# Kernel optimization log

Hardware: AMD Instinct MI355X
Metric: run time of the kernel (lower is better)

The kernel has to match this reference:

```python
import jax, jax.numpy as jnp
import numpy as np

B, S, H, DH = 2, 2048, 12, 64
D = H * DH          # dim_hidden = 768
DF = 4 * D          # dim_ffn = 3072
EPS = 1e-5


def layernorm(x, g, b):
    mu = jnp.mean(x, -1, keepdims=True)
    var = jnp.var(x, -1, keepdims=True)
    return (x - mu) * jax.lax.rsqrt(var + EPS) * g + b


def setup_inputs() -> dict:
    key = jax.random.key(0)
    ks = jax.random.split(key, 8)
    sc = 0.02
    x = jax.random.normal(ks[0], (B, S, D), jnp.float32)
    # causal mask: True where attention is NOT allowed (masked_fill semantics)
    causal = ~jnp.tril(jnp.ones((S, S), dtype=bool))
    attn_mask = jnp.broadcast_to(causal, (B, S, S))
    Wq = jax.random.normal(ks[1], (D, D), jnp.float32) * sc
    Wk = jax.random.normal(ks[2], (D, D), jnp.float32) * sc
    Wv = jax.random.normal(ks[3], (D, D), jnp.float32) * sc
    Wo = jax.random.normal(ks[4], (D, D), jnp.float32) * sc
    bo = jnp.zeros((D,), jnp.float32)
    g1 = jnp.ones((D,), jnp.float32)
    b1 = jnp.zeros((D,), jnp.float32)
    W1 = jax.random.normal(ks[5], (DF, D), jnp.float32) * sc  # conv1 (k=1) == linear
    bb1 = jnp.zeros((DF,), jnp.float32)
    W2 = jax.random.normal(ks[6], (D, DF), jnp.float32) * sc
    bb2 = jnp.zeros((D,), jnp.float32)
    g2 = jnp.ones((D,), jnp.float32)
    b2 = jnp.zeros((D,), jnp.float32)
    return dict(x=x, attn_mask=attn_mask, Wq=Wq, Wk=Wk, Wv=Wv, Wo=Wo, bo=bo,
                g1=g1, b1=b1, W1=W1, bb1=bb1, W2=W2, bb2=bb2, g2=g2, b2=b2)


def reference(x, attn_mask, Wq, Wk, Wv, Wo, bo, g1, b1, W1, bb1, W2, bb2, g2, b2):
    b, s, d = x.shape
    # projections and head split: (B, H, S, DH)
    q = (x @ Wq.T).reshape(b, s, H, DH).transpose(0, 2, 1, 3)
    k = (x @ Wk.T).reshape(b, s, H, DH).transpose(0, 2, 1, 3)
    v = (x @ Wv.T).reshape(b, s, H, DH).transpose(0, 2, 1, 3)
    scores = jnp.einsum('bhqd,bhkd->bhqk', q, k) / jnp.sqrt(jnp.float32(DH))
    scores = jnp.where(attn_mask[:, None, :, :], jnp.float32(-1e9), scores)
    attn_p = jax.nn.softmax(scores, axis=-1)          # (B, H, S, S)
    attn_v = jnp.einsum('bhqk,bhkd->bhqd', attn_p, v)
    attn_v = attn_v.transpose(0, 2, 1, 3).reshape(b, s, d)
    attn_out = attn_v @ Wo.T + bo
    h = layernorm(x + attn_out, g1, b1)
    f = jax.nn.gelu(h @ W1.T + bb1, approximate=False) @ W2.T + bb2
    y = layernorm(h + f, g2, b2)
    return y, attn_p
```

## Files before the change

### kernel.cpp

```cpp
#include <hip/hip_runtime.h>
#include <hip/hip_bf16.h>

#define DEV static __device__ __forceinline__

typedef short bf16x8  __attribute__((ext_vector_type(8)));
typedef short short4v __attribute__((ext_vector_type(4)));
typedef float f32x4   __attribute__((ext_vector_type(4)));

#define MFMA16(a,b,c) __builtin_amdgcn_mfma_f32_16x16x32_bf16((a),(b),(c),0,0,0)

DEV short f2b(float f) {
  unsigned u = __float_as_uint(f);
  unsigned r = (u + 0x7fffu + ((u >> 16) & 1u)) >> 16;
  return (short)r;
}

DEV void gld16(const void* g, void* l) {
  __builtin_amdgcn_global_load_lds(
      (const __attribute__((address_space(1))) unsigned int*)g,
      (__attribute__((address_space(3))) unsigned int*)l, 16, 0, 0);
}

DEV bf16x8 ldfrag(const short* tile, int row, int unit) {
  return *(const bf16x8*)(tile + row * 64 + (((unit) ^ (row & 7)) << 3));
}

__global__ __launch_bounds__(256) void cast4(const float4* __restrict__ in,
                                             short4v* __restrict__ out, int n4) {
  int i = blockIdx.x * 256 + threadIdx.x;
  if (i < n4) {
    float4 v = in[i];
    short4v o;
    o[0] = f2b(v.x); o[1] = f2b(v.y); o[2] = f2b(v.z); o[3] = f2b(v.w);
    out[i] = o;
  }
}

__global__ __launch_bounds__(256) void cast4_m(
    const float4* __restrict__ s0, const float4* __restrict__ s1,
    const float4* __restrict__ s2, const float4* __restrict__ s3,
    short4v* __restrict__ d0, short4v* __restrict__ d1,
    short4v* __restrict__ d2, short4v* __restrict__ d3, int n4) {
  int i = blockIdx.x * 256 + threadIdx.x;
  if (i >= n4) return;
  int b = blockIdx.y;
  const float4* s = (b == 0) ? s0 : (b == 1) ? s1 : (b == 2) ? s2 : s3;
  short4v* d = (b == 0) ? d0 : (b == 1) ? d1 : (b == 2) ? d2 : d3;
  float4 v = s[i];
  short4v o;
  o[0] = f2b(v.x); o[1] = f2b(v.y); o[2] = f2b(v.z); o[3] = f2b(v.w);
  d[i] = o;
}

template <int MODE>
__global__ __launch_bounds__(256) void gemm_nt(
    const short* __restrict__ A, const short* __restrict__ Bw,
    float* __restrict__ outF, short* __restrict__ outB,
    short* __restrict__ outB2, short* __restrict__ outB3,
    const float* __restrict__ bias, int M, int N, int K, int Kstride,
    float scale) {
  __shared__ __align__(16) short As[128 * 64];
  __shared__ __align__(16) short Bs[128 * 64];
  int tid = threadIdx.x;
  int w = tid >> 6, lane = tid & 63, quad = lane >> 4, l15 = lane & 15;
  int m0 = blockIdx.x * 128, n0 = blockIdx.y * 128;
  int kbase = blockIdx.z * K;
  const short* Ap = A + kbase;
  const short* Bp = Bw + kbase;
  int wm = (w & 1) * 64, wn = (w >> 1) * 64;
  f32x4 acc[4][4] = {};

  for (int k0 = 0; k0 < K; k0 += 64) {
    __syncthreads();
#pragma unroll
    for (int i = 0; i < 4; i++) {
      int id = i * 256 + tid;
      int r = id >> 3, u = id & 7;
      int su = u ^ (r & 7);
      gld16(Ap + (size_t)(m0 + r) * Kstride + k0 + su * 8, As + id * 8);
      gld16(Bp + (size_t)(n0 + r) * Kstride + k0 + su * 8, Bs + id * 8);
    }
    __syncthreads();
#pragma unroll
    for (int kk = 0; kk < 2; kk++) {
      bf16x8 af[4], bfr[4];
#pragma unroll
      for (int mt = 0; mt < 4; mt++)
        af[mt] = ldfrag(As, wm + mt * 16 + l15, kk * 4 + quad);
#pragma unroll
      for (int nt = 0; nt < 4; nt++)
        bfr[nt] = ldfrag(Bs, wn + nt * 16 + l15, kk * 4 + quad);
#pragma unroll
      for (int mt = 0; mt < 4; mt++)
#pragma unroll
        for (int nt = 0; nt < 4; nt++)
          acc[mt][nt] = MFMA16(af[mt], bfr[nt], acc[mt][nt]);
    }
  }

  if (MODE == 0) outF += (size_t)blockIdx.z * M * N;

#pragma unroll
  for (int mt = 0; mt < 4; mt++) {
#pragma unroll
    for (int nt = 0; nt < 4; nt++) {
      if (MODE == 4 && n0 >= 1536) {
        int gcol = n0 + wn + nt * 16 + l15;
        int col = gcol - 1536;
        int h_ = col >> 6, d_ = col & 63;
        int srow = m0 + wm + mt * 16 + quad * 4;
        int b_ = srow >> 11, s_ = srow & 2047;
        short4v pk;
#pragma unroll
        for (int reg = 0; reg < 4; reg++) pk[reg] = f2b(acc[mt][nt][reg]);
        *(short4v*)(outB3 + ((size_t)(b_ * 12 + h_) * 64 + d_) * 2048 + s_) = pk;
      } else {
#pragma unroll
        for (int reg = 0; reg < 4; reg++) {
          int grow = m0 + wm + mt * 16 + quad * 4 + reg;
          int gcol = n0 + wn + nt * 16 + l15;
          float v = acc[mt][nt][reg];
          if (MODE == 0) {
            outF[(size_t)grow * N + gcol] = v;
          } else if (MODE == 3) {
            float t = v + bias[gcol];
            float z = t * (1.0f + 0.044715f * t * t);
            float ge = t / (1.0f + __expf(-1.5957691216f * z));
            outB[(size_t)grow * N + gcol] = f2b(ge);
          } else if (MODE == 4) {
            int b_ = grow >> 11, s_ = grow & 2047;
            if (gcol < 768) {
              int h_ = gcol >> 6, d_ = gcol & 63;
              outB[(((size_t)(b_ * 12 + h_) << 11) + s_) * 64 + d_] = f2b(v * scale);
            } else {
              int col = gcol - 768;
              int h_ = col >> 6, d_ = col & 63;
              outB2[(((size_t)(b_ * 12 + h_) << 11) + s_) * 64 + d_] = f2b(v);
            }
          }
        }
      }
    }
  }
}

__global__ __launch_bounds__(256) void attn_kernel(
    const short* __restrict__ Qb, const short* __restrict__ Kb,
    const short* __restrict__ Vtb, float* __restrict__ Pout,
    short* __restrict__ Ov) {
  __shared__ __align__(16) short Qs[64 * 64];
  __shared__ __align__(16) short Ks[64 * 64];
  __shared__ __align__(16) short Vs[64 * 64];
  __shared__ __align__(16) short Ps[4 * 16 * 64];
  int tid = threadIdx.x, w = tid >> 6, lane = tid & 63;
  int quad = lane >> 4, l15 = lane & 15;
  int qb = (gridDim.x - 1) - blockIdx.x;
  int bh = blockIdx.y, q0 = qb << 6;
  const short* qp = Qb + ((size_t)bh << 17);
  const short* kp = Kb + ((size_t)bh << 17);
  const short* vp = Vtb + ((size_t)bh << 17);
  float* pp = Pout + ((size_t)bh << 22);

#pragma unroll
  for (int t = 0; t < 2; t++) {
    int row = t * 32 + w * 8 + (lane >> 3);
    int su = (lane & 7) ^ (row & 7);
    gld16(qp + ((size_t)(q0 + row) << 6) + su * 8, Qs + row * 64 + (lane & 7) * 8);
  }

  float lsum[4] = {0.f, 0.f, 0.f, 0.f};

  for (int kt = 0; kt <= qb; kt++) {
    __syncthreads();
#pragma unroll
    for (int t = 0; t < 2; t++) {
      int row = t * 32 + w * 8 + (lane >> 3);
      int su = (lane & 7) ^ (row & 7);
      gld16(kp + ((size_t)((kt << 6) + row) << 6) + su * 8,
            Ks + row * 64 + (lane & 7) * 8);
    }
    __syncthreads();
    f32x4 sc[4] = {};
    int arow = w * 16 + l15;
    bf16x8 a0 = ldfrag(Qs, arow, quad), a1 = ldfrag(Qs, arow, 4 + quad);
#pragma unroll
    for (int nt = 0; nt < 4; nt++) {
      int brow = nt * 16 + l15;
      bf16x8 b0 = ldfrag(Ks, brow, quad), b1 = ldfrag(Ks, brow, 4 + quad);
      sc[nt] = MFMA16(a0, b0, sc[nt]);
      sc[nt] = MFMA16(a1, b1, sc[nt]);
    }
    if (kt == qb) {
#pragma unroll
      for (int nt = 0; nt < 4; nt++) {
        int key = (kt << 6) + nt * 16 + l15;
#pragma unroll
        for (int reg = 0; reg < 4; reg++) {
          int qg = q0 + w * 16 + quad * 4 + reg;
          if (key > qg) sc[nt][reg] = -1e30f;
        }
      }
    }
#pragma unroll
    for (int reg = 0; reg < 4; reg++)
      lsum[reg] += __expf(sc[0][reg]) + __expf(sc[1][reg]) +
                   __expf(sc[2][reg]) + __expf(sc[3][reg]);
  }

  float rl[4];
#pragma unroll
  for (int reg = 0; reg < 4; reg++) {
    float s = lsum[reg];
#pragma unroll
    for (int xm = 1; xm < 16; xm <<= 1) s += __shfl_xor(s, xm, 64);
    rl[reg] = 1.0f / s;
  }
  f32x4 oacc[4] = {};

  for (int kt = 0; kt <= qb; kt++) {
    __syncthreads();
#pragma unroll
    for (int t = 0; t < 2; t++) {
      int row = t * 32 + w * 8 + (lane >> 3);
      int su = (lane & 7) ^ (row & 7);
      gld16(kp + ((size_t)((kt << 6) + row) << 6) + su * 8,
            Ks + row * 64 + (lane & 7) * 8);
      gld16(vp + (size_t)row * 2048 + (kt << 6) + su * 8,
            Vs + row * 64 + (lane & 7) * 8);
    }
    __syncthreads();
    f32x4 sc[4] = {};
    int arow = w * 16 + l15;
    bf16x8 a0 = ldfrag(Qs, arow, quad), a1 = ldfrag(Qs, arow, 4 + quad);
#pragma unroll
    for (int nt = 0; nt < 4; nt++) {
      int brow = nt * 16 + l15;
      bf16x8 b0 = ldfrag(Ks, brow, quad), b1 = ldfrag(Ks, brow, 4 + quad);
      sc[nt] = MFMA16(a0, b0, sc[nt]);
      sc[nt] = MFMA16(a1, b1, sc[nt]);
    }
    if (kt == qb) {
#pragma unroll
      for (int nt = 0; nt < 4; nt++) {
        int key = (kt << 6) + nt * 16 + l15;
#pragma unroll
        for (int reg = 0; reg < 4; reg++) {
          int qg = q0 + w * 16 + quad * 4 + reg;
          if (key > qg) sc[nt][reg] = -1e30f;
        }
      }
    }
#pragma unroll
    for (int nt = 0; nt < 4; nt++) {
      int key = (kt << 6) + nt * 16 + l15;
#pragma unroll
      for (int reg = 0; reg < 4; reg++) {
        int qg = q0 + w * 16 + quad * 4 + reg;
        float p = __expf(sc[nt][reg]) * rl[reg];
        pp[((size_t)qg << 11) + key] = p;
        int prow = quad * 4 + reg, pcol = nt * 16 + l15;
        Ps[(w << 10) + prow * 64 + (((pcol >> 3) ^ (prow & 7)) << 3) + (pcol & 7)] =
            f2b(p);
      }
    }
    bf16x8 p0 = ldfrag(Ps + (w << 10), l15, quad);
    bf16x8 p1 = ldfrag(Ps + (w << 10), l15, 4 + quad);
#pragma unroll
    for (int dn = 0; dn < 4; dn++) {
      int vrow = dn * 16 + l15;
      bf16x8 v0 = ldfrag(Vs, vrow, quad), v1 = ldfrag(Vs, vrow, 4 + quad);
      oacc[dn] = MFMA16(p0, v0, oacc[dn]);
      oacc[dn] = MFMA16(p1, v1, oacc[dn]);
    }
  }

  int b_ = bh / 12, h_ = bh - b_ * 12;
#pragma unroll
  for (int dn = 0; dn < 4; dn++)
#pragma unroll
    for (int reg = 0; reg < 4; reg++) {
      int s_ = q0 + w * 16 + quad * 4 + reg;
      Ov[(size_t)((b_ << 11) + s_) * 768 + h_ * 64 + dn * 16 + l15] =
          f2b(oacc[dn][reg]);
    }

  int kstart = (qb + 1) << 6;
  if (kstart < 2048) {
    int nch = (2048 - kstart) >> 2;
    for (int r = 0; r < 64; r++) {
      float4* dst = (float4*)(pp + ((size_t)(q0 + r) << 11) + kstart);
      for (int c = tid; c < nch; c += 256) dst[c] = make_float4(0.f, 0.f, 0.f, 0.f);
    }
  }
}

template <int NP>
__global__ __launch_bounds__(256) void ln_fuse(
    const float* __restrict__ p0, const float* __restrict__ p1,
    const float* __restrict__ p2, const float* __restrict__ p3,
    const float* __restrict__ resid, const float* __restrict__ bias,
    const float* __restrict__ gw, const float* __restrict__ bw,
    float* __restrict__ outF, short* __restrict__ outB) {
  int row = blockIdx.x, tid = threadIdx.x;
  size_t off = (size_t)row * 768;
  float v[3];
#pragma unroll
  for (int i = 0; i < 3; i++) {
    int col = tid + i * 256;
    float t = p0[off + col] + resid[off + col] + bias[col];
    if (NP > 1) t += p1[off + col];
    if (NP > 2) t += p2[off + col];
    if (NP > 3) t += p3[off + col];
    v[i] = t;
  }
  float s = v[0] + v[1] + v[2];
  float ss = v[0] * v[0] + v[1] * v[1] + v[2] * v[2];
#pragma unroll
  for (int xm = 1; xm < 64; xm <<= 1) {
    s += __shfl_xor(s, xm, 64);
    ss += __shfl_xor(ss, xm, 64);
  }
  __shared__ float red[8];
  int w = tid >> 6, lane = tid & 63;
  if (lane == 0) { red[w] = s; red[w + 4] = ss; }
  __syncthreads();
  s = red[0] + red[1] + red[2] + red[3];
  ss = red[4] + red[5] + red[6] + red[7];
  float mu = s * (1.0f / 768.0f);
  float var = ss * (1.0f / 768.0f) - mu * mu;
  float inv = rsqrtf(var + 1e-5f);
  float* yF = outF + off;
#pragma unroll
  for (int i = 0; i < 3; i++) {
    int col = tid + i * 256;
    float y = (v[i] - mu) * inv * gw[col] + bw[col];
    yF[col] = y;
    if (outB) outB[off + col] = f2b(y);
  }
}

extern "C" void kernel_launch(void* const* d_in, const int* in_sizes, int n_in,
                              void* d_out, int out_size, void* d_ws, size_t ws_size,
                              hipStream_t stream) {
  const float* x  = (const float*)d_in[0];
  const float* Wq = (const float*)d_in[2];
  const float* Wk = (const float*)d_in[3];
  const float* Wv = (const float*)d_in[4];
  const float* Wo = (const float*)d_in[5];
  const float* bo = (const float*)d_in[6];
  const float* g1 = (const float*)d_in[7];
  const float* b1 = (const float*)d_in[8];
  const float* W1 = (const float*)d_in[9];
  const float* bb1 = (const float*)d_in[10];
  const float* W2 = (const float*)d_in[11];
  const float* bb2 = (const float*)d_in[12];
  const float* g2 = (const float*)d_in[13];
  const float* b2 = (const float*)d_in[14];

  const size_t P = (size_t)4096 * 768;

  char* cur = (char*)d_ws;
  auto take = [&](size_t n) { char* p = cur; cur += (n + 255) & ~(size_t)255; return p; };
  short* xb   = (short*)take(P * 2);
  short* wqkv = (short*)take((size_t)2304 * 768 * 2);
  short* wob  = (short*)take((size_t)589824 * 2);
  short* w1b  = (short*)take((size_t)2359296 * 2);
  short* w2b  = (short*)take((size_t)2359296 * 2);
  short* qbf  = (short*)take(P * 2);
  short* kbf  = (short*)take(P * 2);
  short* vtb  = (short*)take(P * 2);
  short* avb  = (short*)take(P * 2);
  short* hb   = (short*)take(P * 2);
  short* ub   = (short*)take((size_t)4096 * 3072 * 2);
  float* t1   = (float*)take(P * 2 * 4);
  float* hf   = (float*)take(P * 4);
  float* t2   = (float*)take(P * 4 * 4);

  float* y_out = (float*)d_out;
  float* p_out = (float*)d_out + P;

  cast4<<<3072, 256, 0, stream>>>((const float4*)x, (short4v*)xb, 786432);
  cast4_m<<<dim3(576, 4), 256, 0, stream>>>(
      (const float4*)Wq, (const float4*)Wk, (const float4*)Wv, (const float4*)Wo,
      (short4v*)wqkv, (short4v*)(wqkv + 589824), (short4v*)(wqkv + 1179648),
      (short4v*)wob, 147456);
  cast4_m<<<dim3(2304, 2), 256, 0, stream>>>(
      (const float4*)W1, (const float4*)W2, (const float4*)W1, (const float4*)W2,
      (short4v*)w1b, (short4v*)w2b, (short4v*)w1b, (short4v*)w2b, 589824);

  gemm_nt<4><<<dim3(32, 18), 256, 0, stream>>>(
      xb, wqkv, nullptr, qbf, kbf, vtb, nullptr, 4096, 2304, 768, 768, 0.125f);
  attn_kernel<<<dim3(32, 24), 256, 0, stream>>>(qbf, kbf, vtb, p_out, avb);
  gemm_nt<0><<<dim3(32, 6, 2), 256, 0, stream>>>(
      avb, wob, t1, nullptr, nullptr, nullptr, nullptr, 4096, 768, 384, 768, 1.0f);
  ln_fuse<2><<<4096, 256, 0, stream>>>(t1, t1 + P, nullptr, nullptr, x, bo,
                                       g1, b1, hf, hb);
  gemm_nt<3><<<dim3(32, 24), 256, 0, stream>>>(
      hb, w1b, nullptr, ub, nullptr, nullptr, bb1, 4096, 3072, 768, 768, 1.0f);
  gemm_nt<0><<<dim3(32, 6, 4), 256, 0, stream>>>(
      ub, w2b, t2, nullptr, nullptr, nullptr, nullptr, 4096, 768, 768, 3072, 1.0f);
  ln_fuse<4><<<4096, 256, 0, stream>>>(t2, t2 + P, t2 + 2 * P, t2 + 3 * P, hf, bb2,
                                       g2, b2, y_out, nullptr);
}
```

Baseline: 699.3 us.

## Double-buffer LDS tiles in GEMM and attention kernels to overlap loads

Converts the GEMM and both attention passes from single-buffered LDS staging, with two barriers per k-step, to ping-pong buffers. The next tile's global-to-LDS loads are issued before computing on the current tile, and one barrier per iteration remains. This aims to hide global memory latency behind MFMA work and halve barrier count. In exchange the GEMM LDS footprint doubles to 64KB per block and attention LDS grows, which can reduce occupancy.

```diff
diff --git a/kernel.cpp b/kernel.cpp
--- a/kernel.cpp
+++ b/kernel.cpp
@@ -59,8 +59,8 @@
     short* __restrict__ outB2, short* __restrict__ outB3,
     const float* __restrict__ bias, int M, int N, int K, int Kstride,
     float scale) {
-  __shared__ __align__(16) short As[128 * 64];
-  __shared__ __align__(16) short Bs[128 * 64];
+  __shared__ __align__(16) short As[2][128 * 64];
+  __shared__ __align__(16) short Bs[2][128 * 64];
   int tid = threadIdx.x;
   int w = tid >> 6, lane = tid & 63, quad = lane >> 4, l15 = lane & 15;
   int m0 = blockIdx.x * 128, n0 = blockIdx.y * 128;
@@ -70,32 +70,41 @@
   int wm = (w & 1) * 64, wn = (w >> 1) * 64;
   f32x4 acc[4][4] = {};
 
-  for (int k0 = 0; k0 < K; k0 += 64) {
-    __syncthreads();
+  auto stage = [&](int buf, int k0) {
 #pragma unroll
     for (int i = 0; i < 4; i++) {
       int id = i * 256 + tid;
       int r = id >> 3, u = id & 7;
       int su = u ^ (r & 7);
-      gld16(Ap + (size_t)(m0 + r) * Kstride + k0 + su * 8, As + id * 8);
-      gld16(Bp + (size_t)(n0 + r) * Kstride + k0 + su * 8, Bs + id * 8);
-    }
-    __syncthreads();
+      gld16(Ap + (size_t)(m0 + r) * Kstride + k0 + su * 8, &As[buf][id * 8]);
+      gld16(Bp + (size_t)(n0 + r) * Kstride + k0 + su * 8, &Bs[buf][id * 8]);
+    }
+  };
+
+  stage(0, 0);
+  __syncthreads();
+  int cur = 0;
+  for (int k0 = 0; k0 < K; k0 += 64) {
+    if (k0 + 64 < K) stage(cur ^ 1, k0 + 64);
+    const short* as = As[cur];
+    const short* bs = Bs[cur];
 #pragma unroll
     for (int kk = 0; kk < 2; kk++) {
       bf16x8 af[4], bfr[4];
 #pragma unroll
       for (int mt = 0; mt < 4; mt++)
-        af[mt] = ldfrag(As, wm + mt * 16 + l15, kk * 4 + quad);
+        af[mt] = ldfrag(as, wm + mt * 16 + l15, kk * 4 + quad);
 #pragma unroll
       for (int nt = 0; nt < 4; nt++)
-        bfr[nt] = ldfrag(Bs, wn + nt * 16 + l15, kk * 4 + quad);
+        bfr[nt] = ldfrag(bs, wn + nt * 16 + l15, kk * 4 + quad);
 #pragma unroll
       for (int mt = 0; mt < 4; mt++)
 #pragma unroll
         for (int nt = 0; nt < 4; nt++)
           acc[mt][nt] = MFMA16(af[mt], bfr[nt], acc[mt][nt]);
     }
+    __syncthreads();
+    cur ^= 1;
   }
 
   if (MODE == 0) outF += (size_t)blockIdx.z * M * N;
@@ -149,8 +158,8 @@
     const short* __restrict__ Vtb, float* __restrict__ Pout,
     short* __restrict__ Ov) {
   __shared__ __align__(16) short Qs[64 * 64];
-  __shared__ __align__(16) short Ks[64 * 64];
-  __shared__ __align__(16) short Vs[64 * 64];
+  __shared__ __align__(16) short Ks[2][64 * 64];
+  __shared__ __align__(16) short Vs[2][64 * 64];
   __shared__ __align__(16) short Ps[4 * 16 * 64];
   int tid = threadIdx.x, w = tid >> 6, lane = tid & 63;
   int quad = lane >> 4, l15 = lane & 15;
@@ -161,32 +170,47 @@
   const short* vp = Vtb + ((size_t)bh << 17);
   float* pp = Pout + ((size_t)bh << 22);
 
+  auto stageK = [&](int buf, int kt) {
+#pragma unroll
+    for (int t = 0; t < 2; t++) {
+      int row = t * 32 + w * 8 + (lane >> 3);
+      int su = (lane & 7) ^ (row & 7);
+      gld16(kp + ((size_t)((kt << 6) + row) << 6) + su * 8,
+            &Ks[buf][row * 64 + (lane & 7) * 8]);
+    }
+  };
+  auto stageV = [&](int buf, int kt) {
+#pragma unroll
+    for (int t = 0; t < 2; t++) {
+      int row = t * 32 + w * 8 + (lane >> 3);
+      int su = (lane & 7) ^ (row & 7);
+      gld16(vp + (size_t)row * 2048 + (kt << 6) + su * 8,
+            &Vs[buf][row * 64 + (lane & 7) * 8]);
+    }
+  };
+
 #pragma unroll
   for (int t = 0; t < 2; t++) {
     int row = t * 32 + w * 8 + (lane >> 3);
     int su = (lane & 7) ^ (row & 7);
     gld16(qp + ((size_t)(q0 + row) << 6) + su * 8, Qs + row * 64 + (lane & 7) * 8);
   }
+  stageK(0, 0);
+  __syncthreads();
 
   float lsum[4] = {0.f, 0.f, 0.f, 0.f};
+  int cur = 0;
 
   for (int kt = 0; kt <= qb; kt++) {
-    __syncthreads();
-#pragma unroll
-    for (int t = 0; t < 2; t++) {
-      int row = t * 32 + w * 8 + (lane >> 3);
-      int su = (lane & 7) ^ (row & 7);
-      gld16(kp + ((size_t)((kt << 6) + row) << 6) + su * 8,
-            Ks + row * 64 + (lane & 7) * 8);
-    }
-    __syncthreads();
+    if (kt < qb) stageK(cur ^ 1, kt + 1);
     f32x4 sc[4] = {};
     int arow = w * 16 + l15;
     bf16x8 a0 = ldfrag(Qs, arow, quad), a1 = ldfrag(Qs, arow, 4 + quad);
+    const short* ks = Ks[cur];
 #pragma unroll
     for (int nt = 0; nt < 4; nt++) {
       int brow = nt * 16 + l15;
-      bf16x8 b0 = ldfrag(Ks, brow, quad), b1 = ldfrag(Ks, brow, 4 + quad);
+      bf16x8 b0 = ldfrag(ks, brow, quad), b1 = ldfrag(ks, brow, 4 + quad);
       sc[nt] = MFMA16(a0, b0, sc[nt]);
       sc[nt] = MFMA16(a1, b1, sc[nt]);
     }
@@ -205,6 +229,8 @@
     for (int reg = 0; reg < 4; reg++)
       lsum[reg] += __expf(sc[0][reg]) + __expf(sc[1][reg]) +
                    __expf(sc[2][reg]) + __expf(sc[3][reg]);
+    __syncthreads();
+    cur ^= 1;
   }
 
   float rl[4];
@@ -217,25 +243,20 @@
   }
   f32x4 oacc[4] = {};
 
+  stageK(cur, 0);
+  stageV(cur, 0);
+  __syncthreads();
   for (int kt = 0; kt <= qb; kt++) {
-    __syncthreads();
-#pragma unroll
-    for (int t = 0; t < 2; t++) {
-      int row = t * 32 + w * 8 + (lane >> 3);
-      int su = (lane & 7) ^ (row & 7);
-      gld16(kp + ((size_t)((kt << 6) + row) << 6) + su * 8,
-            Ks + row * 64 + (lane & 7) * 8);
-      gld16(vp + (size_t)row * 2048 + (kt << 6) + su * 8,
-            Vs + row * 64 + (lane & 7) * 8);
-    }
-    __syncthreads();
+    if (kt < qb) { stageK(cur ^ 1, kt + 1); stageV(cur ^ 1, kt + 1); }
     f32x4 sc[4] = {};
     int arow = w * 16 + l15;
     bf16x8 a0 = ldfrag(Qs, arow, quad), a1 = ldfrag(Qs, arow, 4 + quad);
+    const short* ks = Ks[cur];
+    const short* vs = Vs[cur];
 #pragma unroll
     for (int nt = 0; nt < 4; nt++) {
       int brow = nt * 16 + l15;
-      bf16x8 b0 = ldfrag(Ks, brow, quad), b1 = ldfrag(Ks, brow, 4 + quad);
+      bf16x8 b0 = ldfrag(ks, brow, quad), b1 = ldfrag(ks, brow, 4 + quad);
       sc[nt] = MFMA16(a0, b0, sc[nt]);
       sc[nt] = MFMA16(a1, b1, sc[nt]);
     }
@@ -268,10 +289,12 @@
 #pragma unroll
     for (int dn = 0; dn < 4; dn++) {
       int vrow = dn * 16 + l15;
-      bf16x8 v0 = ldfrag(Vs, vrow, quad), v1 = ldfrag(Vs, vrow, 4 + quad);
+      bf16x8 v0 = ldfrag(vs, vrow, quad), v1 = ldfrag(vs, vrow, 4 + quad);
       oacc[dn] = MFMA16(p0, v0, oacc[dn]);
       oacc[dn] = MFMA16(p1, v1, oacc[dn]);
     }
+    __syncthreads();
+    cur ^= 1;
   }
 
   int b_ = bh / 12, h_ = bh - b_ * 12;
```

After: 698.0 us. Within noise of the previous version (-0.2%).
